# Performance work log

Measured on AMD Instinct MI355X. Metric: run time of the kernel, lower is better.

## Reference

```python
import jax, jax.numpy as jnp
import numpy as np

WBITS = 4   # weight bits (symmetric signed)
ABITS = 4   # activation bits (unsigned, [0,1])
CBITS = 4   # partial-sum quantization bits
ARRAY = 128 # crossbar array size (input-dim tile)
BN_EPS = 1e-5


def ste_round(x):
    # straight-through estimator round (identity gradient)
    return x + jax.lax.stop_gradient(jnp.round(x) - x)


def setup_inputs() -> dict:
    key = jax.random.key(0)
    k1, k2 = jax.random.split(key)
    B, FIN, FOUT = 65536, 256, 256
    x = jax.random.uniform(k1, (B, FIN), dtype=jnp.float32)        # quantized-act range [0,1]
    weight = jax.random.normal(k2, (FOUT, FIN), dtype=jnp.float32) * 0.05
    gamma = jnp.ones((FOUT,), jnp.float32)
    beta = jnp.zeros((FOUT,), jnp.float32)
    return {"x": x, "weight": weight, "gamma": gamma, "beta": beta}


def reference(x, weight, gamma, beta):
    qmax_w = 2 ** (WBITS - 1) - 1          # 7
    qmax_a = 2 ** ABITS - 1                # 15

    # --- symmetric weight quantization to WBITS (integer levels) ---
    scale_w = jnp.max(jnp.abs(weight)) / qmax_w
    w_int = ste_round(jnp.clip(weight / scale_w, -qmax_w, qmax_w))  # [Fout, Fin]

    # --- unsigned activation quantization to ABITS (integer levels) ---
    x_int = ste_round(jnp.clip(x, 0.0, 1.0) * qmax_a)               # [B, Fin]

    # --- crossbar-tiled integer matmul with partial-sum quantization ---
    B, Fin = x.shape
    Fout = weight.shape[0]
    T = Fin // ARRAY
    xt = x_int.reshape(B, T, ARRAY)          # [B, T, A]
    wt = w_int.reshape(Fout, T, ARRAY)       # [Fout, T, A]
    psum = jnp.einsum('bta,ota->bto', xt, wt)  # integer partial sums, [B, T, Fout]

    # quantize each partial sum to CBITS levels over the full tile dynamic range
    pmax = float(ARRAY * qmax_a * qmax_w)
    step = (2.0 * pmax) / (2 ** CBITS - 1)
    psum_q = ste_round(psum / step) * step

    acc = psum_q.sum(axis=1) * (scale_w / qmax_a)   # dequantized linear output [B, Fout]

    # --- BatchNorm1d (training mode: batch statistics) ---
    mu = acc.mean(axis=0)
    var = acc.var(axis=0)
    y = (acc - mu) * jax.lax.rsqrt(var + BN_EPS) * gamma + beta

    # --- quantized clipped-ReLU activation to ABITS ---
    out = ste_round(jnp.clip(y, 0.0, 1.0) * qmax_a) / qmax_a
    return out
```

## Files before the change

kernel.cpp:

```cpp
#include <hip/hip_runtime.h>
#include <cstdint>
#include <cstddef>

typedef int   v4i __attribute__((ext_vector_type(4)));
typedef float v4f __attribute__((ext_vector_type(4)));

static constexpr int NREP = 16;

static constexpr size_t WQ_OFF    = 0;
static constexpr size_t STATS_OFF = 65536;
static constexpr size_t PART_OFF  = STATS_OFF + NREP*512*4;
static constexpr size_t AB_OFF    = PART_OFF + 256;
static constexpr size_t SBUF_OFF  = 131072 + 2048;
static constexpr size_t WS_NEEDED = SBUF_OFF + (size_t)65536 * 256;

__device__ __forceinline__ int rhe1792(int p) {
    unsigned u = (unsigned)(p + 17024);
    unsigned v = u >> 8;
    unsigned d = (v * 147u) >> 10;
    int q = (int)d - 9;
    unsigned tie = (unsigned)(((u & 255u) | (v - 7u * d)) == 0u);
    q -= (int)(tie & ((unsigned)q & 1u));
    return q;
}

__global__ void k_maxabs(const float* __restrict__ w, float* __restrict__ partials,
                         int* __restrict__ stats) {
    __shared__ float wmax[4];
    int idx = blockIdx.x * 256 + threadIdx.x;
    float4 f = ((const float4*)w)[idx];
    float m = fmaxf(fmaxf(fabsf(f.x), fabsf(f.y)), fmaxf(fabsf(f.z), fabsf(f.w)));
    #pragma unroll
    for (int s = 32; s > 0; s >>= 1) m = fmaxf(m, __shfl_xor(m, s, 64));
    if ((threadIdx.x & 63) == 0) wmax[threadIdx.x >> 6] = m;
    if (idx < NREP * 512) stats[idx] = 0;
    __syncthreads();
    if (threadIdx.x == 0)
        partials[blockIdx.x] = fmaxf(fmaxf(wmax[0], wmax[1]), fmaxf(wmax[2], wmax[3]));
}

__device__ __forceinline__ float reduce_partials(const float* __restrict__ partials, int tid) {
    float p = partials[tid & 63];
    #pragma unroll
    for (int s = 32; s > 0; s >>= 1) p = fmaxf(p, __shfl_xor(p, s, 64));
    return p;
}

__global__ void k_wquant(const float* __restrict__ w, const float* __restrict__ partials,
                         signed char* __restrict__ wq) {
    int idx = blockIdx.x * 256 + threadIdx.x;
    float scale = reduce_partials(partials, threadIdx.x) / 7.0f;
    float4 f = ((const float4*)w)[idx];
    int q0 = (int)rintf(fminf(fmaxf(f.x / scale, -7.f), 7.f));
    int q1 = (int)rintf(fminf(fmaxf(f.y / scale, -7.f), 7.f));
    int q2 = (int)rintf(fminf(fmaxf(f.z / scale, -7.f), 7.f));
    int q3 = (int)rintf(fminf(fmaxf(f.w / scale, -7.f), 7.f));
    ((int*)wq)[idx] = (q0 & 255) | ((q1 & 255) << 8) | ((q2 & 255) << 16) | ((q3 & 255) << 24);
}

template <typename ST>
__global__ __launch_bounds__(512, 4) void k_gemm(
    const float* __restrict__ x, const signed char* __restrict__ wq,
    ST* __restrict__ sbuf, int* __restrict__ stats)
{
    __shared__ __align__(16) signed char ldsx[64 * 272];
    const int tid  = threadIdx.x;
    const int lane = tid & 63;
    const int wv   = tid >> 6;
    const int obase = wv * 32;
    const int lr = lane & 15, quad = lane >> 4;
    const size_t rb0 = (size_t)blockIdx.x * 64;

    v4f f[8];
    const v4f* xb = (const v4f*)(x + rb0 * 256);
    #pragma unroll
    for (int j = 0; j < 8; ++j)
        f[j] = __builtin_nontemporal_load(&xb[j * 512 + tid]);

    v4i wf[2][4];
    #pragma unroll
    for (int ot = 0; ot < 2; ++ot)
        #pragma unroll
        for (int kt = 0; kt < 4; ++kt)
            wf[ot][kt] = *(const v4i*)(wq + (size_t)(obase + ot * 16 + lr) * 256 + kt * 64 + quad * 16);

    #pragma unroll
    for (int j = 0; j < 8; ++j) {
        int idx = j * 512 + tid;
        int row = idx >> 6, c = idx & 63;
        int b0 = (int)rintf(fminf(fmaxf(f[j][0], 0.f), 1.f) * 15.f);
        int b1 = (int)rintf(fminf(fmaxf(f[j][1], 0.f), 1.f) * 15.f);
        int b2 = (int)rintf(fminf(fmaxf(f[j][2], 0.f), 1.f) * 15.f);
        int b3 = (int)rintf(fminf(fmaxf(f[j][3], 0.f), 1.f) * 15.f);
        *(int*)(ldsx + row * 272 + c * 4) = b0 | (b1 << 8) | (b2 << 16) | (b3 << 24);
    }
    __syncthreads();

    int ssum[2] = {0, 0};
    int ssq[2]  = {0, 0};

    #pragma unroll
    for (int t = 0; t < 4; ++t) {
        v4i a[4];
        #pragma unroll
        for (int kt = 0; kt < 4; ++kt)
            a[kt] = *(const v4i*)(ldsx + (t * 16 + lr) * 272 + kt * 64 + quad * 16);
        const size_t rowbase = rb0 + (size_t)t * 16;
        #pragma unroll
        for (int ot = 0; ot < 2; ++ot) {
            v4i acc0 = {0, 0, 0, 0}, acc1 = {0, 0, 0, 0};
            acc0 = __builtin_amdgcn_mfma_i32_16x16x64_i8(a[0], wf[ot][0], acc0, 0, 0, 0);
            acc0 = __builtin_amdgcn_mfma_i32_16x16x64_i8(a[1], wf[ot][1], acc0, 0, 0, 0);
            acc1 = __builtin_amdgcn_mfma_i32_16x16x64_i8(a[2], wf[ot][2], acc1, 0, 0, 0);
            acc1 = __builtin_amdgcn_mfma_i32_16x16x64_i8(a[3], wf[ot][3], acc1, 0, 0, 0);
            ST* sp = sbuf + (rowbase + quad * 4) * 256 + obase + ot * 16 + lr;
            #pragma unroll
            for (int e = 0; e < 4; ++e) {
                int s = rhe1792(acc0[e]) + rhe1792(acc1[e]);
                ssum[ot] += s;
                ssq[ot]  += s * s;
                sp[(size_t)e * 256] = (ST)s;
            }
        }
    }
    int* st = stats + (blockIdx.x & (NREP - 1)) * 512;
    #pragma unroll
    for (int ot = 0; ot < 2; ++ot) {
        int v = ssum[ot], u = ssq[ot];
        v += __shfl_xor(v, 16, 64); v += __shfl_xor(v, 32, 64);
        u += __shfl_xor(u, 16, 64); u += __shfl_xor(u, 32, 64);
        if (quad == 0) {
            atomicAdd(&st[obase + ot * 16 + lr], v);
            atomicAdd(&st[256 + obase + ot * 16 + lr], u);
        }
    }
}

__global__ void k_stats(const int* __restrict__ stats, const float* __restrict__ partials,
                        const float* __restrict__ gamma, const float* __restrict__ beta,
                        float2* __restrict__ AB)
{
    int o = threadIdx.x;
    int s = 0, q = 0;
    #pragma unroll
    for (int rr = 0; rr < NREP; ++rr) {
        s += stats[rr * 512 + o];
        q += stats[rr * 512 + 256 + o];
    }
    float scale_w = reduce_partials(partials, o) / 7.0f;
    float t = scale_w / 15.0f;
    double Cs = 1792.0 * (double)t;
    const double N = 65536.0;
    double mean_s = (double)s / N;
    double var_s  = (double)q / N - mean_s * mean_s;
    double var    = Cs * Cs * var_s;
    double inv    = 1.0 / sqrt(var + 1e-5);
    double A = Cs * inv * (double)gamma[o];
    double B = (double)beta[o] - Cs * mean_s * inv * (double)gamma[o];
    AB[o] = make_float2((float)A, (float)B);
}

template <typename LT>
__global__ __launch_bounds__(256) void k_out(const LT* sbuf, const float2* __restrict__ AB,
                                             float* out)
{
    const int tid = threadIdx.x;
    const int o0 = (tid * 4) & 255;
    const float4 ab01 = *(const float4*)((const float*)AB + 2 * o0);
    const float4 ab23 = *(const float4*)((const float*)AB + 2 * o0 + 4);
    const size_t base = (size_t)blockIdx.x * 1024 + tid;
    #pragma unroll
    for (int j = 0; j < 4; ++j) {
        const size_t F4 = base + (size_t)j * 256;
        float v0, v1, v2, v3;
        if constexpr (sizeof(LT) == 1) {
            int sv = ((const int*)sbuf)[F4];
            v0 = (float)((sv << 24) >> 24);
            v1 = (float)((sv << 16) >> 24);
            v2 = (float)((sv << 8) >> 24);
            v3 = (float)(sv >> 24);
        } else {
            v4f fl = ((const v4f*)sbuf)[F4];
            v0 = fl[0]; v1 = fl[1]; v2 = fl[2]; v3 = fl[3];
        }
        float y0 = rintf(fminf(fmaxf(v0 * ab01.x + ab01.y, 0.f), 1.f) * 15.f);
        float y1 = rintf(fminf(fmaxf(v1 * ab01.z + ab01.w, 0.f), 1.f) * 15.f);
        float y2 = rintf(fminf(fmaxf(v2 * ab23.x + ab23.y, 0.f), 1.f) * 15.f);
        float y3 = rintf(fminf(fmaxf(v3 * ab23.z + ab23.w, 0.f), 1.f) * 15.f);
        const float inv15 = 0.066666666666666666f;
        v4f o = { y0 * inv15, y1 * inv15, y2 * inv15, y3 * inv15 };
        __builtin_nontemporal_store(o, (v4f*)out + F4);
    }
}

extern "C" void kernel_launch(void* const* d_in, const int* in_sizes, int n_in,
                              void* d_out, int out_size, void* d_ws, size_t ws_size,
                              hipStream_t stream)
{
    const float* x     = (const float*)d_in[0];
    const float* w     = (const float*)d_in[1];
    const float* gamma = (const float*)d_in[2];
    const float* beta  = (const float*)d_in[3];
    float* out = (float*)d_out;
    char* ws = (char*)d_ws;

    signed char* wq       = (signed char*)(ws + WQ_OFF);
    int*         stats    = (int*)(ws + STATS_OFF);
    float*       partials = (float*)(ws + PART_OFF);
    float2*      AB       = (float2*)(ws + AB_OFF);

    k_maxabs<<<dim3(64), dim3(256), 0, stream>>>(w, partials, stats);
    k_wquant<<<dim3(64), dim3(256), 0, stream>>>(w, partials, wq);

    if (ws_size >= WS_NEEDED) {
        signed char* sbuf = (signed char*)(ws + SBUF_OFF);
        k_gemm<signed char><<<dim3(1024), dim3(512), 0, stream>>>(x, wq, sbuf, stats);
        k_stats<<<dim3(1), dim3(256), 0, stream>>>(stats, partials, gamma, beta, AB);
        k_out<signed char><<<dim3(4096), dim3(256), 0, stream>>>(sbuf, AB, out);
    } else {
        k_gemm<float><<<dim3(1024), dim3(512), 0, stream>>>(x, wq, out, stats);
        k_stats<<<dim3(1), dim3(256), 0, stream>>>(stats, partials, gamma, beta, AB);
        k_out<float><<<dim3(4096), dim3(256), 0, stream>>>(out, AB, out);
    }
}
```

Measured before the change: 141.3 us.

## Fuse BN stats finalization into output kernel and remap output blocks

Removes the single-block k_stats launch and has every k_out block recompute the per-feature BN scale/shift into shared memory before applying it. It also halves the number of replicated atomic stat buffers, changes the x loads in the GEMM from nontemporal to normal loads, and permutes the order in which k_out blocks visit the output. This removes one kernel launch and its serialization gap, but every one of the 4096 output blocks now does redundant stats reads and double-precision math, and fewer replicas may increase atomic contention.

After: 135.1 us. 4.4% less time.

```diff
diff --git a/kernel.cpp b/kernel.cpp
--- a/kernel.cpp
+++ b/kernel.cpp
@@ -5,12 +5,11 @@
 typedef int   v4i __attribute__((ext_vector_type(4)));
 typedef float v4f __attribute__((ext_vector_type(4)));
 
-static constexpr int NREP = 16;
+static constexpr int NREP = 8;
 
 static constexpr size_t WQ_OFF    = 0;
 static constexpr size_t STATS_OFF = 65536;
 static constexpr size_t PART_OFF  = STATS_OFF + NREP*512*4;
-static constexpr size_t AB_OFF    = PART_OFF + 256;
 static constexpr size_t SBUF_OFF  = 131072 + 2048;
 static constexpr size_t WS_NEEDED = SBUF_OFF + (size_t)65536 * 256;
 
@@ -75,7 +74,7 @@
     const v4f* xb = (const v4f*)(x + rb0 * 256);
     #pragma unroll
     for (int j = 0; j < 8; ++j)
-        f[j] = __builtin_nontemporal_load(&xb[j * 512 + tid]);
+        f[j] = xb[j * 512 + tid];
 
     v4i wf[2][4];
     #pragma unroll
@@ -136,39 +135,42 @@
     }
 }
 
-__global__ void k_stats(const int* __restrict__ stats, const float* __restrict__ partials,
-                        const float* __restrict__ gamma, const float* __restrict__ beta,
-                        float2* __restrict__ AB)
-{
-    int o = threadIdx.x;
-    int s = 0, q = 0;
-    #pragma unroll
-    for (int rr = 0; rr < NREP; ++rr) {
-        s += stats[rr * 512 + o];
-        q += stats[rr * 512 + 256 + o];
-    }
-    float scale_w = reduce_partials(partials, o) / 7.0f;
-    float t = scale_w / 15.0f;
-    double Cs = 1792.0 * (double)t;
-    const double N = 65536.0;
-    double mean_s = (double)s / N;
-    double var_s  = (double)q / N - mean_s * mean_s;
-    double var    = Cs * Cs * var_s;
-    double inv    = 1.0 / sqrt(var + 1e-5);
-    double A = Cs * inv * (double)gamma[o];
-    double B = (double)beta[o] - Cs * mean_s * inv * (double)gamma[o];
-    AB[o] = make_float2((float)A, (float)B);
-}
-
 template <typename LT>
-__global__ __launch_bounds__(256) void k_out(const LT* sbuf, const float2* __restrict__ AB,
+__global__ __launch_bounds__(256) void k_out(const LT* sbuf, const int* __restrict__ stats,
+                                             const float* __restrict__ partials,
+                                             const float* __restrict__ gamma,
+                                             const float* __restrict__ beta,
                                              float* out)
 {
+    __shared__ float2 ab[256];
     const int tid = threadIdx.x;
+    {
+        int o = tid;
+        int s = 0, q = 0;
+        #pragma unroll
+        for (int rr = 0; rr < NREP; ++rr) {
+            s += stats[rr * 512 + o];
+            q += stats[rr * 512 + 256 + o];
+        }
+        float scale_w = reduce_partials(partials, o) / 7.0f;
+        float t = scale_w / 15.0f;
+        double Cs = 1792.0 * (double)t;
+        const double N = 65536.0;
+        double mean_s = (double)s / N;
+        double var_s  = (double)q / N - mean_s * mean_s;
+        double var    = Cs * Cs * var_s;
+        double inv    = 1.0 / sqrt(var + 1e-5);
+        double A = Cs * inv * (double)gamma[o];
+        double B = (double)beta[o] - Cs * mean_s * inv * (double)gamma[o];
+        ab[o] = make_float2((float)A, (float)B);
+    }
+    __syncthreads();
+
+    const int b = blockIdx.x;
+    const int d = ((b & 7) << 2) | ((b >> 3) & 3) | (b & ~31);
     const int o0 = (tid * 4) & 255;
-    const float4 ab01 = *(const float4*)((const float*)AB + 2 * o0);
-    const float4 ab23 = *(const float4*)((const float*)AB + 2 * o0 + 4);
-    const size_t base = (size_t)blockIdx.x * 1024 + tid;
+    const float2 p0 = ab[o0], p1 = ab[o0 + 1], p2 = ab[o0 + 2], p3 = ab[o0 + 3];
+    const size_t base = (size_t)d * 1024 + tid;
     #pragma unroll
     for (int j = 0; j < 4; ++j) {
         const size_t F4 = base + (size_t)j * 256;
@@ -183,10 +185,10 @@
             v4f fl = ((const v4f*)sbuf)[F4];
             v0 = fl[0]; v1 = fl[1]; v2 = fl[2]; v3 = fl[3];
         }
-        float y0 = rintf(fminf(fmaxf(v0 * ab01.x + ab01.y, 0.f), 1.f) * 15.f);
-        float y1 = rintf(fminf(fmaxf(v1 * ab01.z + ab01.w, 0.f), 1.f) * 15.f);
-        float y2 = rintf(fminf(fmaxf(v2 * ab23.x + ab23.y, 0.f), 1.f) * 15.f);
-        float y3 = rintf(fminf(fmaxf(v3 * ab23.z + ab23.w, 0.f), 1.f) * 15.f);
+        float y0 = rintf(fminf(fmaxf(v0 * p0.x + p0.y, 0.f), 1.f) * 15.f);
+        float y1 = rintf(fminf(fmaxf(v1 * p1.x + p1.y, 0.f), 1.f) * 15.f);
+        float y2 = rintf(fminf(fmaxf(v2 * p2.x + p2.y, 0.f), 1.f) * 15.f);
+        float y3 = rintf(fminf(fmaxf(v3 * p3.x + p3.y, 0.f), 1.f) * 15.f);
         const float inv15 = 0.066666666666666666f;
         v4f o = { y0 * inv15, y1 * inv15, y2 * inv15, y3 * inv15 };
         __builtin_nontemporal_store(o, (v4f*)out + F4);
@@ -207,7 +209,6 @@
     signed char* wq       = (signed char*)(ws + WQ_OFF);
     int*         stats    = (int*)(ws + STATS_OFF);
     float*       partials = (float*)(ws + PART_OFF);
-    float2*      AB       = (float2*)(ws + AB_OFF);
 
     k_maxabs<<<dim3(64), dim3(256), 0, stream>>>(w, partials, stats);
     k_wquant<<<dim3(64), dim3(256), 0, stream>>>(w, partials, wq);
@@ -215,11 +216,11 @@
     if (ws_size >= WS_NEEDED) {
         signed char* sbuf = (signed char*)(ws + SBUF_OFF);
         k_gemm<signed char><<<dim3(1024), dim3(512), 0, stream>>>(x, wq, sbuf, stats);
-        k_stats<<<dim3(1), dim3(256), 0, stream>>>(stats, partials, gamma, beta, AB);
-        k_out<signed char><<<dim3(4096), dim3(256), 0, stream>>>(sbuf, AB, out);
+        k_out<signed char><<<dim3(4096), dim3(256), 0, stream>>>(sbuf, stats, partials,
+                                                                 gamma, beta, out);
     } else {
         k_gemm<float><<<dim3(1024), dim3(512), 0, stream>>>(x, wq, out, stats);
-        k_stats<<<dim3(1), dim3(256), 0, stream>>>(stats, partials, gamma, beta, AB);
-        k_out<float><<<dim3(4096), dim3(256), 0, stream>>>(out, AB, out);
-    }
-}
+        k_out<float><<<dim3(4096), dim3(256), 0, stream>>>(out, stats, partials,
+                                                           gamma, beta, out);
+    }
+}
```
